# Optimization experiments

Measured on AMD Instinct MI355X. Metric: run time of the kernel, lower is better.

The kernel has to match this reference:

```python
import jax, jax.numpy as jnp
import numpy as np

N = 65536          # nodes per snapshot
B = 32             # batch
COMP = 2           # components (u, v)
SFC = 2            # number of space-filling-curve orderings
K, S, P = 32, 4, 16  # dimension==2 branch: kernel, stride, padding
CHANNELS = [2, 4, 8, 16, 16, 16]  # per-layer channels (x2 until num_final_channels=16)
NCONV = 5          # conv sizes: 65536->16385->4097->1025->257->65
FINAL_SIZE = 65


def _neigh_idx(n):
    # get_neighbourhood_md(arange(n), gen_neighbour_keys(1), ordering=True):
    # per-node [i-1, i, i+1], clamped at boundaries.
    i = jnp.arange(n)
    return jnp.stack([jnp.clip(i - 1, 0, n - 1), i, jnp.clip(i + 1, 0, n - 1)], axis=-1)


def setup_inputs() -> dict:
    key = jax.random.key(0)
    ks = jax.random.split(key, 16)
    d = {}
    d["x"] = jax.random.normal(ks[0], (B, N, COMP), jnp.float32)
    d["orderings"] = jax.random.randint(ks[1], (SFC, N), 0, N)  # SFC permutations (gather indices)
    d["sp_w"] = jnp.ones((N, 3), jnp.float32) / 3.0  # NearestNeighbouring weights (shared over sfcs)
    d["sp_b"] = jnp.zeros((N,), jnp.float32)
    for j in range(NCONV):
        cin, cout = CHANNELS[j], CHANNELS[j + 1]
        d[f"conv_w{j}"] = jax.random.normal(ks[2 + j], (cout, cin, K), jnp.float32) * (1.0 / np.sqrt(cin * K))
        d[f"conv_b{j}"] = jnp.zeros((cout,), jnp.float32)
    fc_in = SFC * CHANNELS[-1] * FINAL_SIZE  # 2080
    d["fc1_w"] = jax.random.normal(ks[8], (128, fc_in), jnp.float32) * (1.0 / np.sqrt(fc_in))
    d["fc1_b"] = jnp.zeros((128,), jnp.float32)
    d["fc2_w"] = jax.random.normal(ks[9], (16, 128), jnp.float32) * (1.0 / np.sqrt(128))
    d["fc2_b"] = jnp.zeros((16,), jnp.float32)
    return d


def _forward(x, orderings, sp_w, sp_b, conv_ws, conv_bs, fc1_w, fc1_b, fc2_w, fc2_b):
    neigh = _neigh_idx(N)  # (N,3)
    feats = []
    for i in range(SFC):
        a = x[:, orderings[i], :]            # SFC permutation gather -> (B,N,C)
        a = jnp.transpose(a, (0, 2, 1))      # (B,C,N)
        g = a[:, :, neigh]                   # neighbourhood gather -> (B,C,N,3)
        a = jnp.tanh(jnp.einsum('bcnk,nk->bcn', g, sp_w) + sp_b)  # sparse NN combine
        for w, b in zip(conv_ws, conv_bs):
            a = jax.lax.conv_general_dilated(a, w, (S,), [(P, P)],
                                             dimension_numbers=('NCH', 'OIH', 'NCH'))
            a = jnp.tanh(a + b[None, :, None])
        feats.append(a.reshape(a.shape[0], -1))  # (B, 16*65)
    h = jnp.concatenate(feats, axis=-1)          # (B, 2080)
    h = jnp.tanh(h @ fc1_w.T + fc1_b)            # (B, 128)
    h = jnp.tanh(h @ fc2_w.T + fc2_b)            # (B, 16) latent
    return h


def reference(x, orderings, sp_w, sp_b, conv_w0, conv_b0, conv_w1, conv_b1, conv_w2, conv_b2,
              conv_w3, conv_b3, conv_w4, conv_b4, fc1_w, fc1_b, fc2_w, fc2_b):
    conv_ws = [conv_w0, conv_w1, conv_w2, conv_w3, conv_w4]
    conv_bs = [conv_b0, conv_b1, conv_b2, conv_b3, conv_b4]
    return _forward(x, orderings, sp_w, sp_b, conv_ws, conv_bs, fc1_w, fc1_b, fc2_w, fc2_b)
```

## Files before the change

kernel.cpp:

```cpp
#include <hip/hip_runtime.h>
#include <math.h>

#define NPTS 65536

__device__ __forceinline__ float4 ld4_guard(const float* __restrict__ row, int pos, int hi) {
    float4 v;
    if (pos >= 0 && pos + 4 <= hi) {
        v = *(const float4*)(row + pos);
    } else {
        v.x = (pos + 0 >= 0 && pos + 0 < hi) ? row[pos + 0] : 0.f;
        v.y = (pos + 1 >= 0 && pos + 1 < hi) ? row[pos + 1] : 0.f;
        v.z = (pos + 2 >= 0 && pos + 2 < hi) ? row[pos + 2] : 0.f;
        v.w = (pos + 3 >= 0 && pos + 3 < hi) ? row[pos + 3] : 0.f;
    }
    return v;
}

__device__ __forceinline__ int pmap(int p) { return p + ((p >> 5) << 2); }

__global__ __launch_bounds__(256) void transpose_kernel(const float* __restrict__ x,
                                                        float* __restrict__ xt)
{
    __shared__ float tile[64][65];
    int n0 = blockIdx.x * 64;
    int tid = threadIdx.x;
    int lane = tid & 63, w = tid >> 6;
    const float2* x2 = (const float2*)x;
#pragma unroll
    for (int bq = 0; bq < 8; ++bq) {
        int b = bq * 4 + w;
        float2 v = x2[(size_t)b * NPTS + n0 + lane];
        tile[lane][b * 2 + 0] = v.x;
        tile[lane][b * 2 + 1] = v.y;
    }
    __syncthreads();
    int f4 = tid & 15;
#pragma unroll
    for (int rq = 0; rq < 4; ++rq) {
        int r = rq * 16 + (tid >> 4);
        float4 v = make_float4(tile[r][f4 * 4 + 0], tile[r][f4 * 4 + 1],
                               tile[r][f4 * 4 + 2], tile[r][f4 * 4 + 3]);
        *(float4*)&xt[(size_t)(n0 + r) * 64 + f4 * 4] = v;
    }
}

__global__ __launch_bounds__(256) void smooth_kernel(const float* __restrict__ xt,
                                                     const int* __restrict__ ord,
                                                     const float* __restrict__ sp_w,
                                                     const float* __restrict__ sp_b,
                                                     float* __restrict__ s)
{
    __shared__ int s_idx[130];
    __shared__ float rows[130][65];
    int n0 = blockIdx.x * 128;
    int tid = threadIdx.x;
    if (tid < 130) {
        int g = n0 - 1 + tid;
        g = g < 0 ? 0 : (g > NPTS - 1 ? NPTS - 1 : g);
        s_idx[tid] = ord[g];
    }
    __syncthreads();
    for (int q = tid; q < 130 * 16; q += 256) {
        int r = q >> 4, f4 = q & 15;
        float4 v = *(const float4*)&xt[(size_t)s_idx[r] * 64 + f4 * 4];
        rows[r][f4 * 4 + 0] = v.x; rows[r][f4 * 4 + 1] = v.y;
        rows[r][f4 * 4 + 2] = v.z; rows[r][f4 * 4 + 3] = v.w;
    }
    __syncthreads();
    int n_local = tid & 127, half = tid >> 7;
    int n = n0 + n_local;
    float w0 = sp_w[n * 3 + 0], w1 = sp_w[n * 3 + 1], w2 = sp_w[n * 3 + 2];
    float bb = sp_b[n];
#pragma unroll 4
    for (int bc = 0; bc < 64; bc += 2) {
        int bce = bc + half;
        float v = w0 * rows[n_local][bce] + w1 * rows[n_local + 1][bce]
                + w2 * rows[n_local + 2][bce] + bb;
        s[(size_t)bce * NPTS + n] = tanhf(v);
    }
}

__global__ __launch_bounds__(256, 2) void conv0_wpc(
    const float* __restrict__ in,
    const float* __restrict__ w,
    const float* __restrict__ bias,
    float* __restrict__ out)
{
    constexpr int SPAN = 2076;
    __shared__ float in_s[2][2336];

    int bid = blockIdx.x;
    int tile = bid % 33;
    int b = bid / 33;
    int tid = threadIdx.x;

    int base = tile * 2048 - 16;
    const float* inb = in + (size_t)b * 2 * NPTS;
    for (int q = tid; q < 2 * (SPAN / 4); q += 256) {
        int ci = q / (SPAN / 4), fp = q - ci * (SPAN / 4);
        int p = 4 * fp;
        float4 v = ld4_guard(inb + (size_t)ci * NPTS, base + p, NPTS);
        *(float4*)&in_s[ci][pmap(p)] = v;
    }
    __syncthreads();

    int lane = tid & 63;
    int co_u = __builtin_amdgcn_readfirstlane(tid >> 6);

    float acc[8];
    float bv = bias[co_u];
#pragma unroll
    for (int j = 0; j < 8; ++j) acc[j] = bv;

#pragma unroll 1
    for (int ci = 0; ci < 2; ++ci) {
        const float* wb = w + (co_u * 2 + ci) * 32;
        float wv[32];
#pragma unroll
        for (int k = 0; k < 32; ++k) wv[k] = wb[k];
        float4 v[15];
#pragma unroll
        for (int k = 0; k < 15; ++k)
            v[k] = *(const float4*)&in_s[ci][pmap(32 * lane + 4 * k)];
#pragma unroll
        for (int k4 = 0; k4 < 8; ++k4) {
            float wx = wv[4 * k4], wy = wv[4 * k4 + 1], wz = wv[4 * k4 + 2], ww = wv[4 * k4 + 3];
#pragma unroll
            for (int j = 0; j < 8; ++j)
                acc[j] += v[j + k4].x * wx + v[j + k4].y * wy
                        + v[j + k4].z * wz + v[j + k4].w * ww;
        }
    }

    int l0 = tile * 512 + lane * 8;
    size_t row = ((size_t)b * 4 + co_u) * 16388;
    if (l0 + 8 <= 16385) {
        float4 s0 = make_float4(tanhf(acc[0]), tanhf(acc[1]), tanhf(acc[2]), tanhf(acc[3]));
        float4 s1 = make_float4(tanhf(acc[4]), tanhf(acc[5]), tanhf(acc[6]), tanhf(acc[7]));
        *(float4*)&out[row + l0] = s0;
        *(float4*)&out[row + l0 + 4] = s1;
    } else {
#pragma unroll
        for (int j = 0; j < 8; ++j)
            if (l0 + j < 16385) out[row + l0 + j] = tanhf(acc[j]);
    }
}

__global__ __launch_bounds__(512) void conv1_wpc(
    const float* __restrict__ in,
    const float* __restrict__ w,
    const float* __restrict__ bias,
    float* __restrict__ out)
{
    constexpr int SPAN = 1052;
    __shared__ float in_s[4][1184];

    int bid = blockIdx.x;
    int tile = bid % 17;
    int b = bid / 17;
    int tid = threadIdx.x;

    int base = tile * 1024 - 16;
    const float* inb = in + (size_t)b * 4 * 16388;
    for (int q = tid; q < 4 * (SPAN / 4); q += 512) {
        int ci = q / (SPAN / 4), fp = q - ci * (SPAN / 4);
        int p = 4 * fp;
        float4 v = ld4_guard(inb + (size_t)ci * 16388, base + p, 16385);
        *(float4*)&in_s[ci][pmap(p)] = v;
    }
    __syncthreads();

    int lane = tid & 63;
    int co_u = __builtin_amdgcn_readfirstlane(tid >> 6);

    float acc[4];
    float bv = bias[co_u];
#pragma unroll
    for (int j = 0; j < 4; ++j) acc[j] = bv;

#pragma unroll 1
    for (int ci = 0; ci < 4; ++ci) {
        const float* wb = w + (co_u * 4 + ci) * 32;
        float wv[32];
#pragma unroll
        for (int k = 0; k < 32; ++k) wv[k] = wb[k];
        float4 v[11];
#pragma unroll
        for (int k = 0; k < 11; ++k)
            v[k] = *(const float4*)&in_s[ci][pmap(16 * lane + 4 * k)];
#pragma unroll
        for (int k4 = 0; k4 < 8; ++k4) {
            float wx = wv[4 * k4], wy = wv[4 * k4 + 1], wz = wv[4 * k4 + 2], ww = wv[4 * k4 + 3];
#pragma unroll
            for (int j = 0; j < 4; ++j)
                acc[j] += v[j + k4].x * wx + v[j + k4].y * wy
                        + v[j + k4].z * wz + v[j + k4].w * ww;
        }
    }

    int l0 = tile * 256 + lane * 4;
    size_t row = ((size_t)b * 8 + co_u) * 4100;
    if (l0 + 4 <= 4097) {
        float4 s0 = make_float4(tanhf(acc[0]), tanhf(acc[1]), tanhf(acc[2]), tanhf(acc[3]));
        *(float4*)&out[row + l0] = s0;
    } else {
#pragma unroll
        for (int j = 0; j < 4; ++j)
            if (l0 + j < 4097) out[row + l0 + j] = tanhf(acc[j]);
    }
}

__global__ __launch_bounds__(512) void conv23_kernel(
    const float* __restrict__ c1,
    const float* __restrict__ w2, const float* __restrict__ b2,
    const float* __restrict__ w3, const float* __restrict__ b3,
    float* __restrict__ c3out)
{
    __shared__ __align__(16) float ubuf[8192];
    __shared__ __align__(16) float c2s[16][180];
    __shared__ __align__(16) float4 w2s[1024];

    const float4* w3s4 = (const float4*)ubuf;

    int b = blockIdx.x >> 3;
    int t = blockIdx.x & 7;
    int tid = threadIdx.x;

    int l3_0 = t * 33;
    int s2 = 4 * l3_0 - 16;
    int s1 = 4 * s2 - 16;

    for (int q = tid; q < 4096; q += 512) {
        int co = q >> 8, rem = q & 255, ci = rem >> 5, k = rem & 31;
        ((float*)w2s)[(((ci << 3) + (k >> 2)) * 16 + co) * 4 + (k & 3)] = w2[q];
    }
    const float* c1b = c1 + (size_t)b * 8 * 4100;
    for (int q = tid; q < 8 * 167; q += 512) {
        int ci = q / 167, p4 = q - ci * 167;
        float4 v = ld4_guard(c1b + (size_t)ci * 4100, s1 + 4 * p4, 4097);
        *(float4*)&ubuf[ci * 752 + pmap(4 * p4)] = v;
    }
    __syncthreads();

    for (int uq = tid; uq < 640; uq += 512) {
        int i = uq >> 2, qt = uq & 3, c0q = qt * 4;
        int l2 = s2 + i;
        bool valid = (l2 >= 0) && (l2 < 1025);
        float acc[4];
#pragma unroll
        for (int c = 0; c < 4; ++c) acc[c] = b2[c0q + c];
#pragma unroll 1
        for (int ci = 0; ci < 8; ++ci) {
            const float* strow = &ubuf[ci * 752];
            float4 v[8];
#pragma unroll
            for (int k = 0; k < 8; ++k)
                v[k] = *(const float4*)&strow[pmap(4 * i + 4 * k)];
#pragma unroll
            for (int k4 = 0; k4 < 8; ++k4) {
#pragma unroll
                for (int c = 0; c < 4; ++c) {
                    float4 wv = w2s[((ci << 3) + k4) * 16 + c0q + c];
                    acc[c] += v[k4].x * wv.x + v[k4].y * wv.y
                            + v[k4].z * wv.z + v[k4].w * wv.w;
                }
            }
        }
#pragma unroll
        for (int c = 0; c < 4; ++c) c2s[c0q + c][pmap(i)] = valid ? tanhf(acc[c]) : 0.f;
    }
    __syncthreads();

    for (int q = tid; q < 8192; q += 512) ubuf[q] = w3[q];
    __syncthreads();

    for (int q = tid; q < 528; q += 512) {
        int co = q / 33, j = q - co * 33;
        int l3 = l3_0 + j;
        if (l3 < 257) {
            float acc = b3[co];
#pragma unroll 1
            for (int ci = 0; ci < 16; ++ci) {
#pragma unroll
                for (int k4 = 0; k4 < 8; ++k4) {
                    float4 v = *(const float4*)&c2s[ci][pmap(4 * j + 4 * k4)];
                    float4 wv = w3s4[(co * 16 + ci) * 8 + k4];
                    acc += v.x * wv.x + v.y * wv.y + v.z * wv.z + v.w * wv.w;
                }
            }
            c3out[((size_t)b * 16 + co) * 260 + l3] = tanhf(acc);
        }
    }
}

__global__ __launch_bounds__(256) void conv4_kernel(
    const float* __restrict__ c3,
    const float* __restrict__ w4, const float* __restrict__ b4,
    float* __restrict__ feats, int ibase)
{
    __shared__ __align__(16) float st[16][320];
    __shared__ float w4s[8][16][32];
    int b = blockIdx.x >> 1, h = blockIdx.x & 1;
    int tid = threadIdx.x;
    for (int i = tid; i < 8 * 16 * 32; i += 256) ((float*)w4s)[i] = w4[h * 4096 + i];
    const float* c3b = c3 + (size_t)b * 16 * 260;
    for (int q = tid; q < 16 * 72; q += 256) {
        int ci = q / 72, p4 = q - ci * 72;
        float4 v = ld4_guard(c3b + (size_t)ci * 260, 4 * p4 - 16, 257);
        *(float4*)&st[ci][pmap(4 * p4)] = v;
    }
    __syncthreads();
    for (int q = tid; q < 520; q += 256) {
        int co_l = q / 65, l4 = q - co_l * 65;
        int co = h * 8 + co_l;
        float acc = b4[co];
#pragma unroll 1
        for (int ci = 0; ci < 16; ++ci) {
#pragma unroll
            for (int k4 = 0; k4 < 8; ++k4) {
                float4 v = *(const float4*)&st[ci][pmap(4 * l4 + 4 * k4)];
                const float* wk = &w4s[co_l][ci][4 * k4];
                acc += v.x * wk[0] + v.y * wk[1] + v.z * wk[2] + v.w * wk[3];
            }
        }
        feats[(size_t)(b & 31) * 2080 + (size_t)((b >> 5) + ibase) * 1040 + co * 65 + l4]
            = tanhf(acc);
    }
}

__global__ __launch_bounds__(256) void fc1_kernel(const float* __restrict__ h,
                                                  const float* __restrict__ w,
                                                  const float* __restrict__ bias,
                                                  float* __restrict__ out)
{
    int lane = threadIdx.x & 63;
    int wid = blockIdx.x * 4 + (threadIdx.x >> 6);
#pragma unroll
    for (int r = 0; r < 4; ++r) {
        int o = wid + r * 1024;
        int b = o >> 7, j = o & 127;
        const float4* h4 = (const float4*)(h + (size_t)b * 2080);
        const float4* w4 = (const float4*)(w + (size_t)j * 2080);
        float acc = 0.f;
#pragma unroll
        for (int q = 0; q < 8; ++q) {
            float4 a = h4[lane + 64 * q], c = w4[lane + 64 * q];
            acc += a.x * c.x + a.y * c.y + a.z * c.z + a.w * c.w;
        }
        if (lane < 8) {
            float4 a = h4[512 + lane], c = w4[512 + lane];
            acc += a.x * c.x + a.y * c.y + a.z * c.z + a.w * c.w;
        }
        for (int off = 32; off; off >>= 1) acc += __shfl_down(acc, off, 64);
        if (lane == 0) out[b * 128 + j] = tanhf(acc + bias[j]);
    }
}

__global__ __launch_bounds__(256) void fc2_kernel(const float* __restrict__ h,
                                                  const float* __restrict__ w,
                                                  const float* __restrict__ bias,
                                                  float* __restrict__ out)
{
    int lane = threadIdx.x & 63;
    int o = blockIdx.x * 4 + (threadIdx.x >> 6);
    int b = o >> 4, j = o & 15;
    const float* hb = h + (size_t)b * 128;
    const float* wj = w + (size_t)j * 128;
    float acc = hb[lane] * wj[lane] + hb[lane + 64] * wj[lane + 64];
    for (int off = 32; off; off >>= 1) acc += __shfl_down(acc, off, 64);
    if (lane == 0) out[o] = tanhf(acc + bias[j]);
}

extern "C" void kernel_launch(void* const* d_in, const int* in_sizes, int n_in,
                              void* d_out, int out_size, void* d_ws, size_t ws_size,
                              hipStream_t stream)
{
    const float* x = (const float*)d_in[0];
    const int* orderings = (const int*)d_in[1];
    const float* sp_w = (const float*)d_in[2];
    const float* sp_b = (const float*)d_in[3];
    const float* conv_w[5];
    const float* conv_b[5];
    for (int j = 0; j < 5; ++j) {
        conv_w[j] = (const float*)d_in[4 + 2 * j];
        conv_b[j] = (const float*)d_in[5 + 2 * j];
    }
    const float* fc1_w = (const float*)d_in[14];
    const float* fc1_b = (const float*)d_in[15];
    const float* fc2_w = (const float*)d_in[16];
    const float* fc2_b = (const float*)d_in[17];

    float* ws = (float*)d_ws;

    if (ws_size >= 12583936ull * 4ull) {
        size_t o_xt = 0, o_c0 = 0, o_s = 4195328;
        size_t o_c1 = 4195328, o_c3 = 6294528, o_f = 6560768, o_h1 = 6627328;

        transpose_kernel<<<NPTS / 64, 256, 0, stream>>>(x, ws + o_xt);
        smooth_kernel<<<512, 256, 0, stream>>>(ws + o_xt, orderings, sp_w, sp_b, ws + o_s);
        smooth_kernel<<<512, 256, 0, stream>>>(ws + o_xt, orderings + NPTS, sp_w, sp_b,
                                               ws + o_s + 4194304);

        conv0_wpc<<<64 * 33, 256, 0, stream>>>(ws + o_s, conv_w[0], conv_b[0], ws + o_c0);
        conv1_wpc<<<64 * 17, 512, 0, stream>>>(ws + o_c0, conv_w[1], conv_b[1], ws + o_c1);
        conv23_kernel<<<64 * 8, 512, 0, stream>>>(ws + o_c1, conv_w[2], conv_b[2],
                                                  conv_w[3], conv_b[3], ws + o_c3);
        conv4_kernel<<<128, 256, 0, stream>>>(ws + o_c3, conv_w[4], conv_b[4],
                                              ws + o_f, 0);
        fc1_kernel<<<256, 256, 0, stream>>>(ws + o_f, fc1_w, fc1_b, ws + o_h1);
        fc2_kernel<<<128, 256, 0, stream>>>(ws + o_h1, fc2_w, fc2_b, (float*)d_out);
    } else {
        size_t o_xt = 0, o_s = 4194304, o_c0 = 8388608;
        size_t o_c1 = 4194304, o_c3 = 5243904, o_f = 10486272, o_h1 = 10552832;

        transpose_kernel<<<NPTS / 64, 256, 0, stream>>>(x, ws + o_xt);
        for (int i = 0; i < 2; ++i) {
            smooth_kernel<<<512, 256, 0, stream>>>(ws + o_xt, orderings + (size_t)i * NPTS,
                                                   sp_w, sp_b, ws + o_s);
            conv0_wpc<<<32 * 33, 256, 0, stream>>>(ws + o_s, conv_w[0], conv_b[0], ws + o_c0);
            conv1_wpc<<<32 * 17, 512, 0, stream>>>(ws + o_c0, conv_w[1], conv_b[1], ws + o_c1);
            conv23_kernel<<<32 * 8, 512, 0, stream>>>(ws + o_c1, conv_w[2], conv_b[2],
                                                      conv_w[3], conv_b[3], ws + o_c3);
            conv4_kernel<<<64, 256, 0, stream>>>(ws + o_c3, conv_w[4], conv_b[4],
                                                 ws + o_f, i);
        }
        fc1_kernel<<<256, 256, 0, stream>>>(ws + o_f, fc1_w, fc1_b, ws + o_h1);
        fc2_kernel<<<128, 256, 0, stream>>>(ws + o_h1, fc2_w, fc2_b, (float*)d_out);
    }
}
```

Measured before the change: 147.3 us.

## Restructure conv23 to map output channels per wave with scalar weight loads

```diff
diff --git a/kernel.cpp b/kernel.cpp
--- a/kernel.cpp
+++ b/kernel.cpp
@@ -17,6 +17,7 @@
 }
 
 __device__ __forceinline__ int pmap(int p) { return p + ((p >> 5) << 2); }
+__device__ __forceinline__ int pm8(int p) { return p + ((p >> 3) << 2); }
 
 __global__ __launch_bounds__(256) void transpose_kernel(const float* __restrict__ x,
                                                         float* __restrict__ xt)
@@ -216,79 +217,93 @@
     const float* __restrict__ w3, const float* __restrict__ b3,
     float* __restrict__ c3out)
 {
-    __shared__ __align__(16) float ubuf[8192];
-    __shared__ __align__(16) float c2s[16][180];
-    __shared__ __align__(16) float4 w2s[1024];
-
-    const float4* w3s4 = (const float4*)ubuf;
+    __shared__ __align__(16) float st[8][760];
+    __shared__ __align__(16) float c2s[16][236];
 
     int b = blockIdx.x >> 3;
     int t = blockIdx.x & 7;
     int tid = threadIdx.x;
+    int lane = tid & 63;
+    int co_u = __builtin_amdgcn_readfirstlane(tid >> 6);
 
     int l3_0 = t * 33;
     int s2 = 4 * l3_0 - 16;
     int s1 = 4 * s2 - 16;
 
-    for (int q = tid; q < 4096; q += 512) {
-        int co = q >> 8, rem = q & 255, ci = rem >> 5, k = rem & 31;
-        ((float*)w2s)[(((ci << 3) + (k >> 2)) * 16 + co) * 4 + (k & 3)] = w2[q];
-    }
     const float* c1b = c1 + (size_t)b * 8 * 4100;
     for (int q = tid; q < 8 * 167; q += 512) {
         int ci = q / 167, p4 = q - ci * 167;
         float4 v = ld4_guard(c1b + (size_t)ci * 4100, s1 + 4 * p4, 4097);
-        *(float4*)&ubuf[ci * 752 + pmap(4 * p4)] = v;
-    }
-    __syncthreads();
-
-    for (int uq = tid; uq < 640; uq += 512) {
-        int i = uq >> 2, qt = uq & 3, c0q = qt * 4;
-        int l2 = s2 + i;
-        bool valid = (l2 >= 0) && (l2 < 1025);
-        float acc[4];
-#pragma unroll
-        for (int c = 0; c < 4; ++c) acc[c] = b2[c0q + c];
+        *(float4*)&st[ci][pmap(4 * p4)] = v;
+    }
+    __syncthreads();
+
+    {
+        int i0 = 3 * lane;
+        if (i0 < 160) {
+            float acc[2][3];
+            float ba = b2[co_u], bb = b2[co_u + 8];
+#pragma unroll
+            for (int j = 0; j < 3; ++j) { acc[0][j] = ba; acc[1][j] = bb; }
 #pragma unroll 1
-        for (int ci = 0; ci < 8; ++ci) {
-            const float* strow = &ubuf[ci * 752];
-            float4 v[8];
-#pragma unroll
-            for (int k = 0; k < 8; ++k)
-                v[k] = *(const float4*)&strow[pmap(4 * i + 4 * k)];
-#pragma unroll
-            for (int k4 = 0; k4 < 8; ++k4) {
-#pragma unroll
-                for (int c = 0; c < 4; ++c) {
-                    float4 wv = w2s[((ci << 3) + k4) * 16 + c0q + c];
-                    acc[c] += v[k4].x * wv.x + v[k4].y * wv.y
-                            + v[k4].z * wv.z + v[k4].w * wv.w;
+            for (int ci = 0; ci < 8; ++ci) {
+                const float* wa = w2 + (size_t)(co_u * 8 + ci) * 32;
+                const float* wb = w2 + (size_t)((co_u + 8) * 8 + ci) * 32;
+                float4 v[10];
+#pragma unroll
+                for (int k = 0; k < 10; ++k)
+                    v[k] = *(const float4*)&st[ci][pmap(12 * lane + 4 * k)];
+#pragma unroll
+                for (int k4 = 0; k4 < 8; ++k4) {
+                    float4 wva = *(const float4*)(wa + 4 * k4);
+                    float4 wvb = *(const float4*)(wb + 4 * k4);
+#pragma unroll
+                    for (int j = 0; j < 3; ++j) {
+                        acc[0][j] += v[k4 + j].x * wva.x + v[k4 + j].y * wva.y
+                                   + v[k4 + j].z * wva.z + v[k4 + j].w * wva.w;
+                        acc[1][j] += v[k4 + j].x * wvb.x + v[k4 + j].y * wvb.y
+                                   + v[k4 + j].z * wvb.z + v[k4 + j].w * wvb.w;
+                    }
                 }
             }
-        }
-#pragma unroll
-        for (int c = 0; c < 4; ++c) c2s[c0q + c][pmap(i)] = valid ? tanhf(acc[c]) : 0.f;
-    }
-    __syncthreads();
-
-    for (int q = tid; q < 8192; q += 512) ubuf[q] = w3[q];
-    __syncthreads();
-
-    for (int q = tid; q < 528; q += 512) {
-        int co = q / 33, j = q - co * 33;
-        int l3 = l3_0 + j;
+#pragma unroll
+            for (int j = 0; j < 3; ++j) {
+                int i = i0 + j;
+                if (i < 160) {
+                    int l2 = s2 + i;
+                    bool val = (l2 >= 0) && (l2 < 1025);
+                    c2s[co_u][pm8(i)]     = val ? tanhf(acc[0][j]) : 0.f;
+                    c2s[co_u + 8][pm8(i)] = val ? tanhf(acc[1][j]) : 0.f;
+                }
+            }
+        }
+    }
+    __syncthreads();
+
+    if (lane < 33) {
+        int l3 = l3_0 + lane;
         if (l3 < 257) {
-            float acc = b3[co];
+            float acc0 = b3[co_u], acc1 = b3[co_u + 8];
 #pragma unroll 1
             for (int ci = 0; ci < 16; ++ci) {
+                const float* wa = w3 + (size_t)(co_u * 16 + ci) * 32;
+                const float* wb = w3 + (size_t)((co_u + 8) * 16 + ci) * 32;
+                float4 v[8];
+#pragma unroll
+                for (int k = 0; k < 8; ++k)
+                    v[k] = *(const float4*)&c2s[ci][pm8(4 * lane + 4 * k)];
 #pragma unroll
                 for (int k4 = 0; k4 < 8; ++k4) {
-                    float4 v = *(const float4*)&c2s[ci][pmap(4 * j + 4 * k4)];
-                    float4 wv = w3s4[(co * 16 + ci) * 8 + k4];
-                    acc += v.x * wv.x + v.y * wv.y + v.z * wv.z + v.w * wv.w;
+                    float4 wva = *(const float4*)(wa + 4 * k4);
+                    float4 wvb = *(const float4*)(wb + 4 * k4);
+                    acc0 += v[k4].x * wva.x + v[k4].y * wva.y
+                          + v[k4].z * wva.z + v[k4].w * wva.w;
+                    acc1 += v[k4].x * wvb.x + v[k4].y * wvb.y
+                          + v[k4].z * wvb.z + v[k4].w * wvb.w;
                 }
             }
-            c3out[((size_t)b * 16 + co) * 260 + l3] = tanhf(acc);
+            c3out[((size_t)b * 16 + co_u) * 260 + l3] = tanhf(acc0);
+            c3out[((size_t)b * 16 + co_u + 8) * 260 + l3] = tanhf(acc1);
         }
     }
 }
```

After: 150.8 us. 2.3% more time.
